# Kernel optimization log

Hardware: AMD Instinct MI355X
Metric: run time of the kernel (lower is better)

The kernel has to match this reference:

```python
import jax, jax.numpy as jnp
import numpy as np

N_HEAD = 12

def setup_inputs() -> dict:
    key = jax.random.key(0)
    k1, k2, k3 = jax.random.split(key, 3)
    B, T, C = 8, 1024, 768
    x = jax.random.normal(k1, (B, T, C), dtype=jnp.float32)
    W_attn = jax.random.normal(k2, (3 * C, C), dtype=jnp.float32) * 0.02
    b_attn = jax.random.normal(k3, (3 * C,), dtype=jnp.float32) * 0.02
    return {"x": x, "W_attn": W_attn, "b_attn": b_attn}

def reference(x, W_attn, b_attn):
    B, T, C = x.shape
    hd = C // N_HEAD
    # qkv projection: Linear(C, 3C)
    qkv = x @ W_attn.T + b_attn  # (B, T, 3C)
    q, k, v = jnp.split(qkv, 3, axis=-1)
    def to_heads(t):
        return t.reshape(B, T, N_HEAD, hd).transpose(0, 2, 1, 3)  # (B, H, T, hd)
    q, k, v = to_heads(q), to_heads(k), to_heads(v)
    scale = 1.0 / jnp.sqrt(jnp.asarray(hd, dtype=x.dtype))
    att = jnp.einsum('bhqd,bhkd->bhqk', q * scale, k)  # (B, H, T, T)
    causal = jnp.tril(jnp.ones((T, T), dtype=bool))
    # causal mask then ReLU (no softmax)
    att = jnp.where(causal, jnp.maximum(att, 0.0), 0.0)
    y = jnp.einsum('bhqk,bhkd->bhqd', att, v)  # (B, H, T, hd)
    return y.transpose(0, 2, 1, 3).reshape(B, T, C)
```

## Files before the change

kernel.cpp:

```cpp
#include <hip/hip_runtime.h>
#include <hip/hip_bf16.h>
#include <stdint.h>

typedef __attribute__((ext_vector_type(8))) short short8;
typedef __attribute__((ext_vector_type(4))) float f32x4;

#define N_HEADS 12
#define HD      64
#define BSZ     8
#define TSZ     1024
#define CSZ     768
#define MSZ     (BSZ * TSZ)
#define N3      (3 * CSZ)

static __device__ __forceinline__ unsigned short f2bf(float f) {
    union { float f; uint32_t u; } v; v.f = f;
    uint32_t r = v.u + 0x7fffu + ((v.u >> 16) & 1u);
    return (unsigned short)(r >> 16);
}

static __device__ __forceinline__ void gload16(const unsigned short* g,
                                               unsigned short* l) {
    __builtin_amdgcn_global_load_lds(
        (const __attribute__((address_space(1))) void*)g,
        (__attribute__((address_space(3))) void*)l, 16, 0, 0);
}

__global__ void cvt2_f32_to_bf16(const float* __restrict__ x, int nx,
                                 const float* __restrict__ W, int nw,
                                 unsigned short* __restrict__ xb,
                                 unsigned short* __restrict__ wb) {
    int i = (blockIdx.x * blockDim.x + threadIdx.x) * 8;
    const float* s; unsigned short* d; int j;
    if (i < nx) { s = x; d = xb; j = i; }
    else        { s = W; d = wb; j = i - nx; if (j + 7 >= nw) return; }
    float4 f0 = *reinterpret_cast<const float4*>(s + j);
    float4 f1 = *reinterpret_cast<const float4*>(s + j + 4);
    ushort4 u0, u1;
    u0.x = f2bf(f0.x); u0.y = f2bf(f0.y); u0.z = f2bf(f0.z); u0.w = f2bf(f0.w);
    u1.x = f2bf(f1.x); u1.y = f2bf(f1.y); u1.z = f2bf(f1.z); u1.w = f2bf(f1.w);
    *reinterpret_cast<ushort4*>(d + j) = u0;
    *reinterpret_cast<ushort4*>(d + j + 4) = u1;
}

__global__ __launch_bounds__(256, 2) void qkv_gemm(
    const unsigned short* __restrict__ xb,
    const unsigned short* __restrict__ wb,
    const float* __restrict__ bias,
    unsigned short* __restrict__ qo,
    unsigned short* __restrict__ ko,
    unsigned short* __restrict__ vto)
{
    __shared__ unsigned short A0[128 * 64];
    __shared__ unsigned short B0[128 * 64];
    __shared__ unsigned short A1[128 * 64];
    __shared__ unsigned short B1[128 * 64];
    const int tid = threadIdx.x;
    const int lane = tid & 63;
    const int w = tid >> 6;
    const int lr = lane >> 4, lc = lane & 15;
    const int xcd = blockIdx.x & 7, idx = blockIdx.x >> 3;
    const int bm = xcd * 8 + (idx & 7);
    const int bn = idx >> 3;
    const int m0 = bm * 128;
    const int n0 = bn * 128;
    const int wm = (w >> 1) * 64, wn = (w & 1) * 64;

    f32x4 acc[4][4] = {};

#define STAGE(T, LA, LB)                                                   \
    do {                                                                   \
        _Pragma("unroll")                                                  \
        for (int j_ = 0; j_ < 4; ++j_) {                                   \
            int c = j_ * 256 + tid;                                        \
            int r_ = c >> 3;                                               \
            int c8 = ((c & 7) ^ (r_ & 7)) * 8;                             \
            gload16(xb + (size_t)(m0 + r_) * CSZ + (T) * 64 + c8, (LA) + c * 8); \
            gload16(wb + (size_t)(n0 + r_) * CSZ + (T) * 64 + c8, (LB) + c * 8); \
        }                                                                  \
    } while (0)

#define PHASE(T, CA, CB, DO_STAGE, VMN)                                    \
    do {                                                                   \
        short8 af[4][2], bf[4][2];                                         \
        _Pragma("unroll")                                                  \
        for (int mi = 0; mi < 4; ++mi)                                     \
            _Pragma("unroll")                                              \
            for (int ks = 0; ks < 2; ++ks)                                 \
                af[mi][ks] = *reinterpret_cast<const short8*>(             \
                    (CA) + (wm + mi * 16 + lc) * 64 +                      \
                    (((ks * 4 + lr) ^ (lc & 7)) * 8));                     \
        _Pragma("unroll")                                                  \
        for (int ni = 0; ni < 4; ++ni)                                     \
            _Pragma("unroll")                                              \
            for (int ks = 0; ks < 2; ++ks)                                 \
                bf[ni][ks] = *reinterpret_cast<const short8*>(             \
                    (CB) + (wn + ni * 16 + lc) * 64 +                      \
                    (((ks * 4 + lr) ^ (lc & 7)) * 8));                     \
        asm volatile("s_waitcnt lgkmcnt(0)" ::: "memory");                 \
        __builtin_amdgcn_sched_barrier(0);                                 \
        __builtin_amdgcn_s_barrier();          \
        if (DO_STAGE) STAGE((T) + 2, CA, CB);                              \
        __builtin_amdgcn_s_setprio(1);                                     \
        _Pragma("unroll")                                                  \
        for (int ks = 0; ks < 2; ++ks)                                     \
            _Pragma("unroll")                                              \
            for (int mi = 0; mi < 4; ++mi)                                 \
                _Pragma("unroll")                                          \
                for (int ni = 0; ni < 4; ++ni)                             \
                    acc[mi][ni] = __builtin_amdgcn_mfma_f32_16x16x32_bf16( \
                        af[mi][ks], bf[ni][ks], acc[mi][ni], 0, 0, 0);     \
        __builtin_amdgcn_s_setprio(0);                                     \
        asm volatile("s_waitcnt vmcnt(" #VMN ")" ::: "memory");            \
        __builtin_amdgcn_s_barrier();               \
        __builtin_amdgcn_sched_barrier(0);                                 \
    } while (0)

    STAGE(0, A0, B0);
    STAGE(1, A1, B1);
    asm volatile("s_waitcnt vmcnt(8)" ::: "memory");
    __builtin_amdgcn_s_barrier();

    #pragma unroll 1
    for (int tt = 0; tt < 10; tt += 2) {
        PHASE(tt,     A0, B0, true, 8);
        PHASE(tt + 1, A1, B1, true, 8);
    }
    PHASE(10, A0, B0, false, 0);
    PHASE(11, A1, B1, false, 0);
#undef STAGE
#undef PHASE

    const int sec = n0 / CSZ;
    const int nb = n0 - sec * CSZ;
    #pragma unroll
    for (int ni = 0; ni < 4; ++ni) {
        int ncol = wn + ni * 16 + lc;
        int nn = nb + ncol;
        float badd = bias[n0 + ncol];
        int h = nn >> 6, d = nn & 63;
        #pragma unroll
        for (int mi = 0; mi < 4; ++mi) {
            int mbase = m0 + wm + mi * 16 + lr * 4;
            int bb = mbase >> 10, t0 = mbase & 1023;
            int plane = bb * N_HEADS + h;
            if (sec == 0) {
                #pragma unroll
                for (int r = 0; r < 4; ++r)
                    qo[((size_t)plane * TSZ + t0 + r) * HD + d] =
                        f2bf((acc[mi][ni][r] + badd) * 0.125f);
            } else if (sec == 1) {
                #pragma unroll
                for (int r = 0; r < 4; ++r)
                    ko[((size_t)plane * TSZ + t0 + r) * HD + d] =
                        f2bf(acc[mi][ni][r] + badd);
            } else {
                ushort4 pk;
                pk.x = f2bf(acc[mi][ni][0] + badd);
                pk.y = f2bf(acc[mi][ni][1] + badd);
                pk.z = f2bf(acc[mi][ni][2] + badd);
                pk.w = f2bf(acc[mi][ni][3] + badd);
                *reinterpret_cast<ushort4*>(
                    vto + ((size_t)plane * HD + d) * TSZ + t0) = pk;
            }
        }
    }
}

__global__ __launch_bounds__(256, 3) void attn_kernel(
    const unsigned short* __restrict__ q,
    const unsigned short* __restrict__ k,
    const unsigned short* __restrict__ vt,
    float* __restrict__ out)
{
    __shared__ unsigned short Kl[2][64 * 64];
    __shared__ unsigned short Vl[2][64 * 64];
    __shared__ unsigned short Sl[4][32 * 64];
    const int tid = threadIdx.x;
    const int wid = tid >> 6;
    const int lane = tid & 63;
    const int lr = lane >> 4, lc = lane & 15;
    const int xcd = blockIdx.x & 7, slot = blockIdx.x >> 3;
    const int bh = xcd * 12 + (slot >> 3);
    const int pr = 7 - (slot & 7);
    const int jj = pr * 2 + (wid >> 1);
    const int b = bh / N_HEADS, h = bh - b * N_HEADS;
    const size_t base = (size_t)bh * (TSZ * HD);
    const size_t vbase = (size_t)bh * (HD * TSZ);
    const int qrow0 = jj * 64 + (wid & 1) * 32;
    unsigned short* sm = Sl[wid];
    const int ntb = pr * 2 + 2;
    const int ntw = jj + 1;

    short8 aq[2][2];
    #pragma unroll
    for (int ks = 0; ks < 2; ++ks)
        #pragma unroll
        for (int qi = 0; qi < 2; ++qi)
            aq[ks][qi] = *reinterpret_cast<const short8*>(
                q + base + (size_t)(qrow0 + qi * 16 + lc) * HD + ks * 32 + lr * 8);

    f32x4 y[2][4] = {};

#define STAGEKV(KT, BI)                                                     \
    do {                                                                    \
        _Pragma("unroll")                                                   \
        for (int i = 0; i < 2; ++i) {                                       \
            int c = i * 256 + tid;                                          \
            int r_ = c >> 3;                                                \
            int c8 = (c & 7) ^ (r_ & 7);                                    \
            gload16(k + base + (size_t)((KT) * 64 + r_) * HD + c8 * 8,      \
                    Kl[BI] + c * 8);                                        \
            gload16(vt + vbase + (size_t)r_ * TSZ + (KT) * 64 + c8 * 8,     \
                    Vl[BI] + c * 8);                                        \
        }                                                                   \
    } while (0)

    STAGEKV(0, 0);
    __syncthreads();

    for (int kt = 0; kt < ntb; ++kt) {
        const int bi = kt & 1;
        if (kt + 1 < ntb) STAGEKV(kt + 1, bi ^ 1);
        if (kt < ntw) {
            const unsigned short* Kb = Kl[bi];
            const unsigned short* Vb = Vl[bi];
            f32x4 st[4][2] = {};
            #pragma unroll
            for (int ks = 0; ks < 2; ++ks) {
                short8 ak[4];
                #pragma unroll
                for (int ki = 0; ki < 4; ++ki)
                    ak[ki] = *reinterpret_cast<const short8*>(
                        Kb + (ki * 16 + lc) * 64 + (((ks * 4 + lr) ^ (lc & 7)) * 8));
                #pragma unroll
                for (int ki = 0; ki < 4; ++ki)
                    #pragma unroll
                    for (int qi = 0; qi < 2; ++qi)
                        st[ki][qi] = __builtin_amdgcn_mfma_f32_16x16x32_bf16(
                            ak[ki], aq[ks][qi], st[ki][qi], 0, 0, 0);
            }
            const bool diag = (kt == jj);
            const int kv0 = kt * 64;
            #pragma unroll
            for (int ki = 0; ki < 4; ++ki) {
                #pragma unroll
                for (int qi = 0; qi < 2; ++qi) {
                    float vv[4];
                    #pragma unroll
                    for (int r = 0; r < 4; ++r) {
                        float s = fmaxf(st[ki][qi][r], 0.0f);
                        if (diag && (kv0 + ki * 16 + lr * 4 + r > qrow0 + qi * 16 + lc))
                            s = 0.0f;
                        vv[r] = s;
                    }
                    __hip_bfloat162 p0 = __float22bfloat162_rn(make_float2(vv[0], vv[1]));
                    __hip_bfloat162 p1 = __float22bfloat162_rn(make_float2(vv[2], vv[3]));
                    uint2 pk;
                    pk.x = *reinterpret_cast<unsigned*>(&p0);
                    pk.y = *reinterpret_cast<unsigned*>(&p1);
                    int row = qi * 16 + lc;
                    int chunk = (2 * ki + (lr >> 1)) ^ (row & 7);
                    *reinterpret_cast<uint2*>(
                        sm + row * 64 + chunk * 8 + (lr & 1) * 4) = pk;
                }
            }
            #pragma unroll
            for (int ks = 0; ks < 2; ++ks) {
                short8 as[2], bv[4];
                #pragma unroll
                for (int qi = 0; qi < 2; ++qi)
                    as[qi] = *reinterpret_cast<const short8*>(
                        sm + (qi * 16 + lc) * 64 + (((ks * 4 + lr) ^ (lc & 7)) * 8));
                #pragma unroll
                for (int di = 0; di < 4; ++di)
                    bv[di] = *reinterpret_cast<const short8*>(
                        Vb + (di * 16 + lc) * 64 + (((ks * 4 + lr) ^ (lc & 7)) * 8));
                #pragma unroll
                for (int qi = 0; qi < 2; ++qi)
                    #pragma unroll
                    for (int di = 0; di < 4; ++di)
                        y[qi][di] = __builtin_amdgcn_mfma_f32_16x16x32_bf16(
                            as[qi], bv[di], y[qi][di], 0, 0, 0);
            }
        }
        __syncthreads();
    }
#undef STAGEKV

    #pragma unroll
    for (int qi = 0; qi < 2; ++qi)
        #pragma unroll
        for (int di = 0; di < 4; ++di)
            #pragma unroll
            for (int r = 0; r < 4; ++r) {
                int t = qrow0 + qi * 16 + lr * 4 + r;
                int d = di * 16 + lc;
                out[((size_t)b * TSZ + t) * CSZ + h * HD + d] = y[qi][di][r];
            }
}

extern "C" void kernel_launch(void* const* d_in, const int* in_sizes, int n_in,
                              void* d_out, int out_size, void* d_ws, size_t ws_size,
                              hipStream_t stream) {
    const float* x    = (const float*)d_in[0];
    const float* W    = (const float*)d_in[1];
    const float* bias = (const float*)d_in[2];
    float* out = (float*)d_out;

    unsigned short* xb  = (unsigned short*)d_ws;
    unsigned short* wb  = xb + (size_t)MSZ * CSZ;
    unsigned short* qo  = wb + (size_t)N3 * CSZ;
    unsigned short* ko  = qo + (size_t)MSZ * CSZ;
    unsigned short* vto = ko + (size_t)MSZ * CSZ;

    const int nx = MSZ * CSZ;
    const int nw = N3 * CSZ;
    cvt2_f32_to_bf16<<<(nx + nw) / 2048, 256, 0, stream>>>(x, nx, W, nw, xb, wb);
    qkv_gemm<<<dim3(1152), 256, 0, stream>>>(xb, wb, bias, qo, ko, vto);
    attn_kernel<<<dim3(768), 256, 0, stream>>>(qo, ko, vto, out);
}
```

Measured before the change: 89.34 us.

## Deepen K/V prefetch to two tiles with register-staged operands and fine-grained waits

Stages two K/V tiles ahead instead of one. Each tile's K and V fragments are loaded into registers before a barrier, so the same LDS buffer can be refilled with the tile two steps ahead while the MFMAs run. Full __syncthreads calls are replaced with explicit vmcnt waits plus s_barrier, and s_setprio is raised around the MFMA blocks. This is meant to hide global-load latency better, at the cost of more registers and some fragility in the hand-counted vmcnt values.

```diff
diff --git a/kernel.cpp b/kernel.cpp
--- a/kernel.cpp
+++ b/kernel.cpp
@@ -217,29 +217,44 @@
     } while (0)
 
     STAGEKV(0, 0);
-    __syncthreads();
+    STAGEKV(1, 1);
+    asm volatile("s_waitcnt vmcnt(4)" ::: "memory");
+    __builtin_amdgcn_s_barrier();
 
     for (int kt = 0; kt < ntb; ++kt) {
         const int bi = kt & 1;
-        if (kt + 1 < ntb) STAGEKV(kt + 1, bi ^ 1);
-        if (kt < ntw) {
-            const unsigned short* Kb = Kl[bi];
-            const unsigned short* Vb = Vl[bi];
-            f32x4 st[4][2] = {};
-            #pragma unroll
-            for (int ks = 0; ks < 2; ++ks) {
-                short8 ak[4];
-                #pragma unroll
-                for (int ki = 0; ki < 4; ++ki)
-                    ak[ki] = *reinterpret_cast<const short8*>(
+        const bool comp = (kt < ntw);
+        const bool st2 = (kt + 2 < ntb);
+        const unsigned short* Kb = Kl[bi];
+        const unsigned short* Vb = Vl[bi];
+        short8 ak[2][4], bv[2][4];
+        if (comp) {
+            #pragma unroll
+            for (int ks = 0; ks < 2; ++ks)
+                #pragma unroll
+                for (int ki = 0; ki < 4; ++ki) {
+                    ak[ks][ki] = *reinterpret_cast<const short8*>(
                         Kb + (ki * 16 + lc) * 64 + (((ks * 4 + lr) ^ (lc & 7)) * 8));
+                    bv[ks][ki] = *reinterpret_cast<const short8*>(
+                        Vb + (ki * 16 + lc) * 64 + (((ks * 4 + lr) ^ (lc & 7)) * 8));
+                }
+        }
+        asm volatile("s_waitcnt lgkmcnt(0)" ::: "memory");
+        __builtin_amdgcn_sched_barrier(0);
+        __builtin_amdgcn_s_barrier();
+        if (st2) STAGEKV(kt + 2, bi);
+        if (comp) {
+            f32x4 stf[4][2] = {};
+            __builtin_amdgcn_s_setprio(1);
+            #pragma unroll
+            for (int ks = 0; ks < 2; ++ks)
                 #pragma unroll
                 for (int ki = 0; ki < 4; ++ki)
                     #pragma unroll
                     for (int qi = 0; qi < 2; ++qi)
-                        st[ki][qi] = __builtin_amdgcn_mfma_f32_16x16x32_bf16(
-                            ak[ki], aq[ks][qi], st[ki][qi], 0, 0, 0);
-            }
+                        stf[ki][qi] = __builtin_amdgcn_mfma_f32_16x16x32_bf16(
+                            ak[ks][ki], aq[ks][qi], stf[ki][qi], 0, 0, 0);
+            __builtin_amdgcn_s_setprio(0);
             const bool diag = (kt == jj);
             const int kv0 = kt * 64;
             #pragma unroll
@@ -249,7 +264,7 @@
                     float vv[4];
                     #pragma unroll
                     for (int r = 0; r < 4; ++r) {
-                        float s = fmaxf(st[ki][qi][r], 0.0f);
+                        float s = fmaxf(stf[ki][qi][r], 0.0f);
                         if (diag && (kv0 + ki * 16 + lr * 4 + r > qrow0 + qi * 16 + lc))
                             s = 0.0f;
                         vv[r] = s;
@@ -267,24 +282,27 @@
             }
             #pragma unroll
             for (int ks = 0; ks < 2; ++ks) {
-                short8 as[2], bv[4];
+                short8 as[2];
                 #pragma unroll
                 for (int qi = 0; qi < 2; ++qi)
                     as[qi] = *reinterpret_cast<const short8*>(
                         sm + (qi * 16 + lc) * 64 + (((ks * 4 + lr) ^ (lc & 7)) * 8));
-                #pragma unroll
-                for (int di = 0; di < 4; ++di)
-                    bv[di] = *reinterpret_cast<const short8*>(
-                        Vb + (di * 16 + lc) * 64 + (((ks * 4 + lr) ^ (lc & 7)) * 8));
+                __builtin_amdgcn_s_setprio(1);
                 #pragma unroll
                 for (int qi = 0; qi < 2; ++qi)
                     #pragma unroll
                     for (int di = 0; di < 4; ++di)
                         y[qi][di] = __builtin_amdgcn_mfma_f32_16x16x32_bf16(
-                            as[qi], bv[di], y[qi][di], 0, 0, 0);
+                            as[qi], bv[ks][di], y[qi][di], 0, 0, 0);
+                __builtin_amdgcn_s_setprio(0);
             }
         }
-        __syncthreads();
+        if (kt + 1 < ntb) {
+            if (st2) asm volatile("s_waitcnt vmcnt(4)" ::: "memory");
+            else     asm volatile("s_waitcnt vmcnt(0)" ::: "memory");
+            __builtin_amdgcn_s_barrier();
+            __builtin_amdgcn_sched_barrier(0);
+        }
     }
 #undef STAGEKV
 
```

New measurement: 107.2 us. +20.0%, slower.

## Use eight waves per block in QKV GEMM with 64x32 warp tiles

Applied to the files above, without the earlier changes.

The QKV projection GEMM block grows from 256 to 512 threads, so eight waves each compute a 64x32 sub-tile instead of four waves each computing 64x64. Each thread now issues four global-to-LDS loads per stage instead of eight, and the vmcnt waits are adjusted to match. The goal is more waves per CU to hide latency, with fewer accumulator registers per wave. In exchange, each wave does less MFMA work per LDS fragment read, so LDS read traffic per FLOP rises, and barrier cost grows with more waves.

```diff
diff --git a/kernel.cpp b/kernel.cpp
--- a/kernel.cpp
+++ b/kernel.cpp
@@ -43,7 +43,7 @@
     *reinterpret_cast<ushort4*>(d + j + 4) = u1;
 }
 
-__global__ __launch_bounds__(256, 2) void qkv_gemm(
+__global__ __launch_bounds__(512, 2) void qkv_gemm(
     const unsigned short* __restrict__ xb,
     const unsigned short* __restrict__ wb,
     const float* __restrict__ bias,
@@ -64,39 +64,41 @@
     const int bn = idx >> 3;
     const int m0 = bm * 128;
     const int n0 = bn * 128;
-    const int wm = (w >> 1) * 64, wn = (w & 1) * 64;
-
-    f32x4 acc[4][4] = {};
+    const int wrow = (w >> 2) * 64;
+    const int wcol = (w & 3) * 32;
+
+    const int r1 = tid >> 3, c1 = ((tid & 7) ^ (r1 & 7)) * 8;
+    const int r2 = 64 + r1,  c2 = ((tid & 7) ^ (r2 & 7)) * 8;
+
+    f32x4 acc[4][2] = {};
 
 #define STAGE(T, LA, LB)                                                   \
     do {                                                                   \
-        _Pragma("unroll")                                                  \
-        for (int j_ = 0; j_ < 4; ++j_) {                                   \
-            int c = j_ * 256 + tid;                                        \
-            int r_ = c >> 3;                                               \
-            int c8 = ((c & 7) ^ (r_ & 7)) * 8;                             \
-            gload16(xb + (size_t)(m0 + r_) * CSZ + (T) * 64 + c8, (LA) + c * 8); \
-            gload16(wb + (size_t)(n0 + r_) * CSZ + (T) * 64 + c8, (LB) + c * 8); \
-        }                                                                  \
+        gload16(xb + (size_t)(m0 + r1) * CSZ + (T) * 64 + c1, (LA) + tid * 8); \
+        gload16(xb + (size_t)(m0 + r2) * CSZ + (T) * 64 + c2, (LA) + 4096 + tid * 8); \
+        gload16(wb + (size_t)(n0 + r1) * CSZ + (T) * 64 + c1, (LB) + tid * 8); \
+        gload16(wb + (size_t)(n0 + r2) * CSZ + (T) * 64 + c2, (LB) + 4096 + tid * 8); \
     } while (0)
 
 #define PHASE(T, CA, CB, DO_STAGE, VMN)                                    \
     do {                                                                   \
-        short8 af[4][2], bf[4][2];                                         \
+        short8 af[4][2], bf[2][2];                                         \
         _Pragma("unroll")                                                  \
         for (int mi = 0; mi < 4; ++mi)                                     \
             _Pragma("unroll")                                              \
-            for (int ks = 0; ks < 2; ++ks)                                 \
+            for (int ks = 0; ks < 2; ++ks) {                               \
+                int row = wrow + mi * 16 + lc;                             \
                 af[mi][ks] = *reinterpret_cast<const short8*>(             \
-                    (CA) + (wm + mi * 16 + lc) * 64 +                      \
-                    (((ks * 4 + lr) ^ (lc & 7)) * 8));                     \
+                    (CA) + row * 64 + (((ks * 4 + lr) ^ (row & 7)) * 8));  \
+            }                                                              \
         _Pragma("unroll")                                                  \
-        for (int ni = 0; ni < 4; ++ni)                                     \
+        for (int ni = 0; ni < 2; ++ni)                                     \
             _Pragma("unroll")                                              \
-            for (int ks = 0; ks < 2; ++ks)                                 \
+            for (int ks = 0; ks < 2; ++ks) {                               \
+                int row = wcol + ni * 16 + lc;                             \
                 bf[ni][ks] = *reinterpret_cast<const short8*>(             \
-                    (CB) + (wn + ni * 16 + lc) * 64 +                      \
-                    (((ks * 4 + lr) ^ (lc & 7)) * 8));                     \
+                    (CB) + row * 64 + (((ks * 4 + lr) ^ (row & 7)) * 8));  \
+            }                                                              \
         asm volatile("s_waitcnt lgkmcnt(0)" ::: "memory");                 \
         __builtin_amdgcn_sched_barrier(0);                                 \
         __builtin_amdgcn_s_barrier();          \
@@ -107,7 +109,7 @@
             _Pragma("unroll")                                              \
             for (int mi = 0; mi < 4; ++mi)                                 \
                 _Pragma("unroll")                                          \
-                for (int ni = 0; ni < 4; ++ni)                             \
+                for (int ni = 0; ni < 2; ++ni)                             \
                     acc[mi][ni] = __builtin_amdgcn_mfma_f32_16x16x32_bf16( \
                         af[mi][ks], bf[ni][ks], acc[mi][ni], 0, 0, 0);     \
         __builtin_amdgcn_s_setprio(0);                                     \
@@ -118,13 +120,13 @@
 
     STAGE(0, A0, B0);
     STAGE(1, A1, B1);
-    asm volatile("s_waitcnt vmcnt(8)" ::: "memory");
+    asm volatile("s_waitcnt vmcnt(4)" ::: "memory");
     __builtin_amdgcn_s_barrier();
 
     #pragma unroll 1
     for (int tt = 0; tt < 10; tt += 2) {
-        PHASE(tt,     A0, B0, true, 8);
-        PHASE(tt + 1, A1, B1, true, 8);
+        PHASE(tt,     A0, B0, true, 4);
+        PHASE(tt + 1, A1, B1, true, 4);
     }
     PHASE(10, A0, B0, false, 0);
     PHASE(11, A1, B1, false, 0);
@@ -134,14 +136,14 @@
     const int sec = n0 / CSZ;
     const int nb = n0 - sec * CSZ;
     #pragma unroll
-    for (int ni = 0; ni < 4; ++ni) {
-        int ncol = wn + ni * 16 + lc;
+    for (int ni = 0; ni < 2; ++ni) {
+        int ncol = wcol + ni * 16 + lc;
         int nn = nb + ncol;
         float badd = bias[n0 + ncol];
         int h = nn >> 6, d = nn & 63;
         #pragma unroll
         for (int mi = 0; mi < 4; ++mi) {
-            int mbase = m0 + wm + mi * 16 + lr * 4;
+            int mbase = m0 + wrow + mi * 16 + lr * 4;
             int bb = mbase >> 10, t0 = mbase & 1023;
             int plane = bb * N_HEADS + h;
             if (sec == 0) {
@@ -317,6 +319,6 @@
     const int nx = MSZ * CSZ;
     const int nw = N3 * CSZ;
     cvt2_f32_to_bf16<<<(nx + nw) / 2048, 256, 0, stream>>>(x, nx, W, nw, xb, wb);
-    qkv_gemm<<<dim3(1152), 256, 0, stream>>>(xb, wb, bias, qo, ko, vto);
+    qkv_gemm<<<dim3(1152), 512, 0, stream>>>(xb, wb, bias, qo, ko, vto);
     attn_kernel<<<dim3(768), 256, 0, stream>>>(qo, ko, vto, out);
 }
```

After: 86.47 us. 3.2% less time.
